# Kernel optimization log

Measured on AMD Instinct MI355X. Metric: run time of the kernel, lower is better.

## Reference

```python
import jax, jax.numpy as jnp
import numpy as np


def setup_inputs() -> dict:
    key = jax.random.key(0)
    k1, k2, k3, k4, k5 = jax.random.split(key, 5)
    B, D, H, W, C = 2, 16, 16, 16, 256
    x = jax.random.normal(k1, (B, D, H, W, C), dtype=jnp.float32)
    Wf = jax.random.normal(k2, (C, C // 4), dtype=jnp.float32) * (1.0 / np.sqrt(C))
    Wg = jax.random.normal(k3, (C, C // 4), dtype=jnp.float32) * (1.0 / np.sqrt(C))
    Wh = jax.random.normal(k4, (C, C), dtype=jnp.float32) * (1.0 / np.sqrt(C))
    gamma = jax.random.normal(k5, (1,), dtype=jnp.float32) * 0.1
    return {"x": x, "Wf": Wf, "Wg": Wg, "Wh": Wh, "gamma": gamma}


def reference(x, Wf, Wg, Wh, gamma):
    B, D, H, W, C = x.shape
    N = D * H * W
    xf = x.reshape(B, N, C)  # hw_flatten of input (1x1x1 conv == per-position matmul)
    f = jnp.einsum('bnc,cf->bnf', xf, Wf)   # [B, N, C//4]
    g = jnp.einsum('bnc,cf->bnf', xf, Wg)   # [B, N, C//4]
    h = jnp.einsum('bnc,cf->bnf', xf, Wh)   # [B, N, C]
    s = jnp.einsum('bnf,bmf->bnm', g, f)    # g @ f^T, [B, N, N]
    beta = jax.nn.softmax(s, axis=-1)
    o = jnp.einsum('bnm,bmc->bnc', beta, h)  # [B, N, C]
    out = gamma * o.reshape(B, D, H, W, C) + x
    beta_out = beta.reshape(-1, D, H, W, 1)  # [B*N, D, H, W, 1] as in original
    return (out, beta_out)
```

## Files before the change

### kernel.cpp

```cpp
#include <hip/hip_runtime.h>

#define NPOS 4096
#define CDIM 256
#define FDIM 64

typedef short short8 __attribute__((ext_vector_type(8)));
typedef float f32x4 __attribute__((ext_vector_type(4)));

__device__ __forceinline__ unsigned short f2bf(float v) {
  unsigned u = __float_as_uint(v);
  unsigned r = (u + 0x7fffu + ((u >> 16) & 1u)) >> 16;
  return (unsigned short)r;
}
__device__ __forceinline__ float bf2f(unsigned short u) {
  return __uint_as_float((unsigned)u << 16);
}
__device__ __forceinline__ short8 as_s8(uint4 u) {
  return *reinterpret_cast<short8*>(&u);
}
__device__ __forceinline__ void gload_lds16(const void* g, void* l) {
  __builtin_amdgcn_global_load_lds(
      (const __attribute__((address_space(1))) unsigned int*)g,
      (__attribute__((address_space(3))) unsigned int*)l, 16, 0, 0);
}

__global__ __launch_bounds__(256) void proj_kernel(
    const float* __restrict__ x, const float* __restrict__ Wf,
    const float* __restrict__ Wg, const float* __restrict__ Wh,
    unsigned short* __restrict__ f_hi, unsigned short* __restrict__ f_lo,
    unsigned short* __restrict__ g_hi, unsigned short* __restrict__ g_lo,
    unsigned short* __restrict__ h_t, float* __restrict__ out) {
  __shared__ float xs[16][CDIM];
  const int row0 = blockIdx.x * 16;
  const int t = threadIdx.x;
  {
    const float4* xv = reinterpret_cast<const float4*>(x + (size_t)row0 * CDIM);
    float4* sv = reinterpret_cast<float4*>(&xs[0][0]);
    float4* ov = reinterpret_cast<float4*>(out + (size_t)row0 * CDIM);
#pragma unroll
    for (int i = 0; i < 4; ++i) {
      const float4 v = xv[t + 256 * i];
      sv[t + 256 * i] = v;
      ov[t + 256 * i] = v;
    }
  }
  __syncthreads();
  {
    float acc[16];
#pragma unroll
    for (int r = 0; r < 16; ++r) acc[r] = 0.f;
    for (int k = 0; k < CDIM; k += 4) {
      const float w0 = Wh[(size_t)(k + 0) * CDIM + t];
      const float w1 = Wh[(size_t)(k + 1) * CDIM + t];
      const float w2 = Wh[(size_t)(k + 2) * CDIM + t];
      const float w3 = Wh[(size_t)(k + 3) * CDIM + t];
#pragma unroll
      for (int r = 0; r < 16; ++r) {
        const float4 xv = *reinterpret_cast<const float4*>(&xs[r][k]);
        float a = acc[r];
        a = fmaf(xv.x, w0, a);
        a = fmaf(xv.y, w1, a);
        a = fmaf(xv.z, w2, a);
        a = fmaf(xv.w, w3, a);
        acc[r] = a;
      }
    }
    const int b = row0 >> 12;
    const int lr = row0 & (NPOS - 1);
    unsigned wd[8];
#pragma unroll
    for (int i = 0; i < 8; ++i)
      wd[i] = (unsigned)f2bf(acc[2 * i]) | ((unsigned)f2bf(acc[2 * i + 1]) << 16);
    uint4* base = reinterpret_cast<uint4*>(h_t + ((size_t)(b * CDIM + t)) * NPOS);
    const int m = t & 7;
    const int c0 = lr >> 3;
    base[c0 ^ m] = make_uint4(wd[0], wd[1], wd[2], wd[3]);
    base[(c0 + 1) ^ m] = make_uint4(wd[4], wd[5], wd[6], wd[7]);
  }
  {
    const int col = t & 63;
    const int rb = (t >> 6) * 4;
    const int colq = col >> 3, cwi = col & 7;
    float af[4] = {0.f, 0.f, 0.f, 0.f};
    float ag[4] = {0.f, 0.f, 0.f, 0.f};
    for (int k = 0; k < CDIM; k += 4) {
      const float wf0 = Wf[(size_t)(k + 0) * FDIM + col];
      const float wf1 = Wf[(size_t)(k + 1) * FDIM + col];
      const float wf2 = Wf[(size_t)(k + 2) * FDIM + col];
      const float wf3 = Wf[(size_t)(k + 3) * FDIM + col];
      const float wg0 = Wg[(size_t)(k + 0) * FDIM + col];
      const float wg1 = Wg[(size_t)(k + 1) * FDIM + col];
      const float wg2 = Wg[(size_t)(k + 2) * FDIM + col];
      const float wg3 = Wg[(size_t)(k + 3) * FDIM + col];
#pragma unroll
      for (int r = 0; r < 4; ++r) {
        const float4 xv = *reinterpret_cast<const float4*>(&xs[rb + r][k]);
        float a = af[r], bb = ag[r];
        a = fmaf(xv.x, wf0, a); a = fmaf(xv.y, wf1, a);
        a = fmaf(xv.z, wf2, a); a = fmaf(xv.w, wf3, a);
        bb = fmaf(xv.x, wg0, bb); bb = fmaf(xv.y, wg1, bb);
        bb = fmaf(xv.z, wg2, bb); bb = fmaf(xv.w, wg3, bb);
        af[r] = a; ag[r] = bb;
      }
    }
#pragma unroll
    for (int r = 0; r < 4; ++r) {
      const int row = row0 + rb + r;
      const int ph = ((colq ^ (row & 7)) << 3) | cwi;
      const size_t of = (size_t)row * FDIM + ph;
      const size_t og = (size_t)row * FDIM + col;
      const unsigned short fh = f2bf(af[r]);
      const unsigned short gh = f2bf(ag[r]);
      f_hi[of] = fh;
      f_lo[of] = f2bf(af[r] - bf2f(fh));
      g_hi[og] = gh;
      g_lo[og] = f2bf(ag[r] - bf2f(gh));
    }
  }
}

__global__ __launch_bounds__(1024, 4) void qk_l_kernel(
    const unsigned short* __restrict__ f_hi, const unsigned short* __restrict__ f_lo,
    const unsigned short* __restrict__ g_hi, const unsigned short* __restrict__ g_lo,
    unsigned short* __restrict__ Pws, float* __restrict__ lrow) {
  __shared__ uint4 Fh[2][256][8];
  __shared__ uint4 Fl[2][256][8];
  __shared__ float partl[16][32];

  const int wg = blockIdx.x;
  const int wgid = (wg & 7) * 32 + (wg >> 3);
  const int b = wgid >> 7;
  const int row0 = (wgid & 127) * 32;
  const int t = threadIdx.x;
  const int w = t >> 6;
  const int l = t & 63;
  const int lr = l & 15;
  const int lk = l >> 4;

  short8 gh0[2], gl0[2], gh1[2], gl1[2];
  {
    const unsigned short* gH0 = g_hi + ((size_t)(b * NPOS + row0 + lr)) * FDIM + lk * 8;
    const unsigned short* gL0 = g_lo + ((size_t)(b * NPOS + row0 + lr)) * FDIM + lk * 8;
    const unsigned short* gH1 = gH0 + (size_t)16 * FDIM;
    const unsigned short* gL1 = gL0 + (size_t)16 * FDIM;
#pragma unroll
    for (int ks = 0; ks < 2; ++ks) {
      gh0[ks] = *reinterpret_cast<const short8*>(gH0 + ks * 32);
      gl0[ks] = *reinterpret_cast<const short8*>(gL0 + ks * 32);
      gh1[ks] = *reinterpret_cast<const short8*>(gH1 + ks * 32);
      gl1[ks] = *reinterpret_cast<const short8*>(gL1 + ks * 32);
    }
  }
  const unsigned short* fbh = f_hi + (size_t)b * NPOS * FDIM;
  const unsigned short* fbl = f_lo + (size_t)b * NPOS * FDIM;
  unsigned short* prow0 = Pws + (size_t)(b * NPOS + row0 + lr) * NPOS;
  unsigned short* prow1 = prow0 + (size_t)16 * NPOS;
  const int rsw = lr & 7;
  float lsum0 = 0.f, lsum1 = 0.f;

#define STAGEA(buf, tile)                                                      \
  do {                                                                         \
    _Pragma("unroll")                                                          \
    for (int j = 0; j < 2; ++j) {                                              \
      const int slot_ = j * 1024 + t;                                          \
      const int row_ = slot_ >> 3, ch_ = slot_ & 7;                            \
      gload_lds16(fbh + (size_t)((tile) * 256 + row_) * FDIM + ch_ * 8,        \
                  (char*)&Fh[buf][0][0] + (size_t)slot_ * 16);                 \
      gload_lds16(fbl + (size_t)((tile) * 256 + row_) * FDIM + ch_ * 8,        \
                  (char*)&Fl[buf][0][0] + (size_t)slot_ * 16);                 \
    }                                                                          \
  } while (0)

  STAGEA(0, 0);
  asm volatile("s_waitcnt vmcnt(0) lgkmcnt(0)\ns_barrier" ::: "memory");

  const int rrA = w * 16 + lr;
  const int fsw = rrA & 7;
  int buf = 0;
  for (int tile = 0; tile < 16; ++tile) {
    if (tile < 15) STAGEA(buf ^ 1, tile + 1);
    __builtin_amdgcn_sched_barrier(0);
    const uint4 h0 = Fh[buf][rrA][lk ^ fsw];
    const uint4 h1 = Fh[buf][rrA][(lk + 4) ^ fsw];
    const uint4 q0 = Fl[buf][rrA][lk ^ fsw];
    const uint4 q1 = Fl[buf][rrA][(lk + 4) ^ fsw];
    {
      f32x4 acca = {0.f, 0.f, 0.f, 0.f};
      f32x4 accb = {0.f, 0.f, 0.f, 0.f};
      acca = __builtin_amdgcn_mfma_f32_16x16x32_bf16(as_s8(h0), gh0[0], acca, 0, 0, 0);
      accb = __builtin_amdgcn_mfma_f32_16x16x32_bf16(as_s8(h0), gl0[0], accb, 0, 0, 0);
      acca = __builtin_amdgcn_mfma_f32_16x16x32_bf16(as_s8(q0), gh0[0], acca, 0, 0, 0);
      accb = __builtin_amdgcn_mfma_f32_16x16x32_bf16(as_s8(h1), gh0[1], accb, 0, 0, 0);
      acca = __builtin_amdgcn_mfma_f32_16x16x32_bf16(as_s8(q1), gh0[1], acca, 0, 0, 0);
      accb = __builtin_amdgcn_mfma_f32_16x16x32_bf16(as_s8(h1), gl0[1], accb, 0, 0, 0);
      const f32x4 acc = acca + accb;
      const int cq = tile * 256 + w * 16 + lk * 4;
      const float e0 = __expf(acc[0]);
      const float e1 = __expf(acc[1]);
      const float e2 = __expf(acc[2]);
      const float e3 = __expf(acc[3]);
      lsum0 += (e0 + e1) + (e2 + e3);
      uint2 pk;
      pk.x = (unsigned)f2bf(e0) | ((unsigned)f2bf(e1) << 16);
      pk.y = (unsigned)f2bf(e2) | ((unsigned)f2bf(e3) << 16);
      const int sidx = (((cq >> 3) ^ rsw) << 3) | (cq & 7);
      *reinterpret_cast<uint2*>(prow0 + sidx) = pk;
    }
    {
      f32x4 acca = {0.f, 0.f, 0.f, 0.f};
      f32x4 accb = {0.f, 0.f, 0.f, 0.f};
      acca = __builtin_amdgcn_mfma_f32_16x16x32_bf16(as_s8(h0), gh1[0], acca, 0, 0, 0);
      accb = __builtin_amdgcn_mfma_f32_16x16x32_bf16(as_s8(h0), gl1[0], accb, 0, 0, 0);
      acca = __builtin_amdgcn_mfma_f32_16x16x32_bf16(as_s8(q0), gh1[0], acca, 0, 0, 0);
      accb = __builtin_amdgcn_mfma_f32_16x16x32_bf16(as_s8(h1), gh1[1], accb, 0, 0, 0);
      acca = __builtin_amdgcn_mfma_f32_16x16x32_bf16(as_s8(q1), gh1[1], acca, 0, 0, 0);
      accb = __builtin_amdgcn_mfma_f32_16x16x32_bf16(as_s8(h1), gl1[1], accb, 0, 0, 0);
      const f32x4 acc = acca + accb;
      const int cq = tile * 256 + w * 16 + lk * 4;
      const float e0 = __expf(acc[0]);
      const float e1 = __expf(acc[1]);
      const float e2 = __expf(acc[2]);
      const float e3 = __expf(acc[3]);
      lsum1 += (e0 + e1) + (e2 + e3);
      uint2 pk;
      pk.x = (unsigned)f2bf(e0) | ((unsigned)f2bf(e1) << 16);
      pk.y = (unsigned)f2bf(e2) | ((unsigned)f2bf(e3) << 16);
      const int sidx = (((cq >> 3) ^ rsw) << 3) | (cq & 7);
      *reinterpret_cast<uint2*>(prow1 + sidx) = pk;
    }
    asm volatile("s_waitcnt vmcnt(2) lgkmcnt(0)\ns_barrier" ::: "memory");
    buf ^= 1;
  }
#undef STAGEA

  lsum0 += __shfl_xor(lsum0, 16);
  lsum0 += __shfl_xor(lsum0, 32);
  lsum1 += __shfl_xor(lsum1, 16);
  lsum1 += __shfl_xor(lsum1, 32);
  if (l < 16) {
    partl[w][l] = lsum0;
    partl[w][16 + l] = lsum1;
  }
  __syncthreads();
  if (t < 32) {
    float s = 0.f;
#pragma unroll
    for (int q = 0; q < 16; ++q) s += partl[q][t];
    lrow[(size_t)b * NPOS + row0 + t] = s;
  }
}

__global__ __launch_bounds__(1024, 4) void pv_split_kernel(
    const unsigned short* __restrict__ h_t, const unsigned short* __restrict__ Pws,
    const float* __restrict__ lrow, const float* __restrict__ gamma,
    float* __restrict__ beta, float* __restrict__ out, float* __restrict__ opart) {
  __shared__ uint4 Ab[2][64][8];
  __shared__ uint4 Bb[2][256][8];
  __shared__ float linvB[64];

  const int wg = blockIdx.x;
  const int wgid = (wg & 7) * 32 + (wg >> 3);
  const int b = wgid >> 7;
  const int khalf = (wgid >> 6) & 1;
  const int row0 = (wgid & 63) * 64;
  const int t = threadIdx.x;
  const int w = t >> 6;
  const int l = t & 63;
  const int lr = l & 15;
  const int lk = l >> 4;

  if (t < 64) linvB[t] = __frcp_rn(lrow[(size_t)b * NPOS + row0 + t]);

  const size_t hoff = (size_t)b * CDIM * NPOS;
  const unsigned short* Pb = Pws + (size_t)(b * NPOS + row0) * NPOS;
  const int kbase = khalf * 256;

#define STAGEB(bufi, kt)                                                        \
  do {                                                                          \
    _Pragma("unroll")                                                           \
    for (int j = 0; j < 2; ++j) {                                               \
      const int slot_ = j * 1024 + t;                                           \
      const int col_ = slot_ >> 3, ch_ = slot_ & 7;                             \
      const unsigned short* g_ = h_t + hoff + (size_t)col_ * NPOS +             \
                                 (size_t)(kbase + (kt) * 8 + ch_) * 8;          \
      gload_lds16(g_, (char*)&Bb[bufi][0][0] + (size_t)slot_ * 16);             \
    }                                                                           \
    if (t < 512) {                                                              \
      const int row_ = t >> 3, ch_ = t & 7;                                     \
      const unsigned short* g_ = Pb + (size_t)row_ * NPOS +                     \
                                 (size_t)(kbase + (kt) * 8 + ch_) * 8;          \
      gload_lds16(g_, (char*)&Ab[bufi][0][0] + (size_t)t * 16);                 \
    }                                                                           \
  } while (0)

  f32x4 acc0 = {0.f, 0.f, 0.f, 0.f}, acc1 = {0.f, 0.f, 0.f, 0.f};
  f32x4 acc2 = {0.f, 0.f, 0.f, 0.f}, acc3 = {0.f, 0.f, 0.f, 0.f};
  const int wrB = w & 3;
  const int wcB = w >> 2;
  const int arB = wrB * 16 + lr;
  const int c0 = wcB * 64 + lr;
  const int c1 = c0 + 16;
  const int c2 = c0 + 32;
  const int c3 = c0 + 48;
  const int brow = t >> 4;
  const int jj = t & 15;

  STAGEB(0, 0);
  asm volatile("s_waitcnt vmcnt(0) lgkmcnt(0)\ns_barrier" ::: "memory");
  const float il_brow = linvB[brow];

  int buf = 0;
  for (int kt = 0; kt < 32; ++kt) {
    if (kt < 31) STAGEB(buf ^ 1, kt + 1);
    __builtin_amdgcn_sched_barrier(0);
    {
      const uint4 a0 = Ab[buf][arB][lk ^ (arB & 7)];
      const uint4 a1 = Ab[buf][arB][(4 + lk) ^ (arB & 7)];
      const uint4 b00 = Bb[buf][c0][lk ^ (c0 & 7)];
      const uint4 b01 = Bb[buf][c1][lk ^ (c1 & 7)];
      const uint4 b02 = Bb[buf][c2][lk ^ (c2 & 7)];
      const uint4 b03 = Bb[buf][c3][lk ^ (c3 & 7)];
      acc0 = __builtin_amdgcn_mfma_f32_16x16x32_bf16(as_s8(a0), as_s8(b00), acc0, 0, 0, 0);
      acc1 = __builtin_amdgcn_mfma_f32_16x16x32_bf16(as_s8(a0), as_s8(b01), acc1, 0, 0, 0);
      acc2 = __builtin_amdgcn_mfma_f32_16x16x32_bf16(as_s8(a0), as_s8(b02), acc2, 0, 0, 0);
      acc3 = __builtin_amdgcn_mfma_f32_16x16x32_bf16(as_s8(a0), as_s8(b03), acc3, 0, 0, 0);
      const uint4 b10 = Bb[buf][c0][(4 + lk) ^ (c0 & 7)];
      const uint4 b11 = Bb[buf][c1][(4 + lk) ^ (c1 & 7)];
      const uint4 b12 = Bb[buf][c2][(4 + lk) ^ (c2 & 7)];
      const uint4 b13 = Bb[buf][c3][(4 + lk) ^ (c3 & 7)];
      acc0 = __builtin_amdgcn_mfma_f32_16x16x32_bf16(as_s8(a1), as_s8(b10), acc0, 0, 0, 0);
      acc1 = __builtin_amdgcn_mfma_f32_16x16x32_bf16(as_s8(a1), as_s8(b11), acc1, 0, 0, 0);
      acc2 = __builtin_amdgcn_mfma_f32_16x16x32_bf16(as_s8(a1), as_s8(b12), acc2, 0, 0, 0);
      acc3 = __builtin_amdgcn_mfma_f32_16x16x32_bf16(as_s8(a1), as_s8(b13), acc3, 0, 0, 0);
    }
    {
      const uint4 u4 = Ab[buf][brow][(jj >> 1) ^ (brow & 7)];
      const uint2 u = (jj & 1) ? make_uint2(u4.z, u4.w) : make_uint2(u4.x, u4.y);
      float4 v;
      v.x = bf2f((unsigned short)(u.x & 0xffffu)) * il_brow;
      v.y = bf2f((unsigned short)(u.x >> 16)) * il_brow;
      v.z = bf2f((unsigned short)(u.y & 0xffffu)) * il_brow;
      v.w = bf2f((unsigned short)(u.y >> 16)) * il_brow;
      *reinterpret_cast<float4*>(beta + (size_t)(b * NPOS + row0 + brow) * NPOS +
                                 khalf * 2048 + kt * 64 + jj * 4) = v;
    }
    asm volatile("s_waitcnt vmcnt(1) lgkmcnt(0)\ns_barrier" ::: "memory");
    buf ^= 1;
  }
#undef STAGEB

  const float gam = gamma[0];
  if (opart) {
    float* op = opart + (size_t)khalf * 2 * NPOS * CDIM;
#pragma unroll
    for (int r = 0; r < 4; ++r) {
      const int lrr = wrB * 16 + lk * 4 + r;
      const int orow = row0 + lrr;
      const float sc = gam * linvB[lrr];
      float* o = op + ((size_t)b * NPOS + orow) * CDIM + wcB * 64 + lr;
      o[0] = sc * acc0[r];
      o[16] = sc * acc1[r];
      o[32] = sc * acc2[r];
      o[48] = sc * acc3[r];
    }
  } else {
#pragma unroll
    for (int r = 0; r < 4; ++r) {
      const int lrr = wrB * 16 + lk * 4 + r;
      const int orow = row0 + lrr;
      const float sc = gam * linvB[lrr];
      float* o = out + ((size_t)b * NPOS + orow) * CDIM + wcB * 64 + lr;
      atomicAdd(o, sc * acc0[r]);
      atomicAdd(o + 16, sc * acc1[r]);
      atomicAdd(o + 32, sc * acc2[r]);
      atomicAdd(o + 48, sc * acc3[r]);
    }
  }
}

__global__ __launch_bounds__(256) void reduce_out_kernel(
    const float* __restrict__ x, const float* __restrict__ opart,
    float* __restrict__ out) {
  const size_t i = ((size_t)blockIdx.x * 256 + threadIdx.x) * 4;
  const float4 xv = *reinterpret_cast<const float4*>(x + i);
  const float4 a = *reinterpret_cast<const float4*>(opart + i);
  const float4 bq = *reinterpret_cast<const float4*>(opart + (size_t)2 * NPOS * CDIM + i);
  float4 r;
  r.x = xv.x + a.x + bq.x;
  r.y = xv.y + a.y + bq.y;
  r.z = xv.z + a.z + bq.z;
  r.w = xv.w + a.w + bq.w;
  *reinterpret_cast<float4*>(out + i) = r;
}

__global__ __launch_bounds__(1024, 4) void attn_fused_kernel(
    const unsigned short* __restrict__ f_hi, const unsigned short* __restrict__ f_lo,
    const unsigned short* __restrict__ g_hi, const unsigned short* __restrict__ g_lo,
    const unsigned short* __restrict__ h_t, const float* __restrict__ x,
    const float* __restrict__ gamma, float* __restrict__ beta,
    float* __restrict__ out) {
  __shared__ __align__(16) char shraw[110592];
  __shared__ float partl[16][16];
  __shared__ float linvs[32];
  uint4 (*Fh)[128][8] = reinterpret_cast<uint4(*)[128][8]>(shraw);
  uint4 (*Fl)[128][8] = reinterpret_cast<uint4(*)[128][8]>(shraw + 32768);
  uint4 (*Ab)[32][8] = reinterpret_cast<uint4(*)[32][8]>(shraw);
  uint4 (*Bb)[256][8] = reinterpret_cast<uint4(*)[256][8]>(shraw + 12288);

  const int wg = blockIdx.x;
  const int wgid = (wg & 7) * 32 + (wg >> 3);
  const int b = wgid >> 7;
  const int row0 = (wgid & 127) * 32;
  const int t = threadIdx.x;
  const int w = t >> 6;
  const int l = t & 63;
  const int lr = l & 15;
  const int lk = l >> 4;

  const int wr = w >> 3;
  const int wq = w & 7;
  const int arow = row0 + wr * 16 + lr;
  short8 gh[2], gl[2];
  {
    const unsigned short* gH = g_hi + ((size_t)(b * NPOS + arow)) * FDIM + lk * 8;
    const unsigned short* gL = g_lo + ((size_t)(b * NPOS + arow)) * FDIM + lk * 8;
#pragma unroll
    for (int ks = 0; ks < 2; ++ks) {
      gh[ks] = *reinterpret_cast<const short8*>(gH + ks * 32);
      gl[ks] = *reinterpret_cast<const short8*>(gL + ks * 32);
    }
  }
  const unsigned short* fbh = f_hi + (size_t)b * NPOS * FDIM;
  const unsigned short* fbl = f_lo + (size_t)b * NPOS * FDIM;
  unsigned short* Pb = (unsigned short*)(beta + (size_t)b * NPOS * NPOS);
  unsigned short* prow = Pb + (size_t)arow * (2 * NPOS) + NPOS;
  const int rsw = lr & 7;
  float lsum = 0.f;
  const int srow_ = t >> 3, sch_ = t & 7;

#define STAGEA(buf, tile)                                                      \
  do {                                                                         \
    const int tr_ = (tile) * 128 + srow_;                                      \
    gload_lds16(fbh + (size_t)tr_ * FDIM + sch_ * 8,                           \
                (char*)&Fh[buf][0][0] + (size_t)t * 16);                       \
    gload_lds16(fbl + (size_t)tr_ * FDIM + sch_ * 8,                           \
                (char*)&Fl[buf][0][0] + (size_t)t * 16);                       \
  } while (0)

  STAGEA(0, 0);
  asm volatile("s_waitcnt vmcnt(0) lgkmcnt(0)\ns_barrier" ::: "memory");

  const int rrA = wq * 16 + lr;
  const int fsw = rrA & 7;
  int buf = 0;
  for (int tile = 0; tile < 32; ++tile) {
    if (tile < 31) STAGEA(buf ^ 1, tile + 1);
    __builtin_amdgcn_sched_barrier(0);
    const uint4 h0 = Fh[buf][rrA][lk ^ fsw];
    const uint4 h1 = Fh[buf][rrA][(lk + 4) ^ fsw];
    const uint4 q0 = Fl[buf][rrA][lk ^ fsw];
    const uint4 q1 = Fl[buf][rrA][(lk + 4) ^ fsw];
    f32x4 acca = {0.f, 0.f, 0.f, 0.f};
    f32x4 accb = {0.f, 0.f, 0.f, 0.f};
    acca = __builtin_amdgcn_mfma_f32_16x16x32_bf16(as_s8(h0), gh[0], acca, 0, 0, 0);
    accb = __builtin_amdgcn_mfma_f32_16x16x32_bf16(as_s8(h0), gl[0], accb, 0, 0, 0);
    acca = __builtin_amdgcn_mfma_f32_16x16x32_bf16(as_s8(q0), gh[0], acca, 0, 0, 0);
    accb = __builtin_amdgcn_mfma_f32_16x16x32_bf16(as_s8(h1), gh[1], accb, 0, 0, 0);
    acca = __builtin_amdgcn_mfma_f32_16x16x32_bf16(as_s8(q1), gh[1], acca, 0, 0, 0);
    accb = __builtin_amdgcn_mfma_f32_16x16x32_bf16(as_s8(h1), gl[1], accb, 0, 0, 0);
    const f32x4 acc = acca + accb;
    const int cq = tile * 128 + wq * 16 + lk * 4;
    const float e0 = __expf(acc[0]);
    const float e1 = __expf(acc[1]);
    const float e2 = __expf(acc[2]);
    const float e3 = __expf(acc[3]);
    lsum += (e0 + e1) + (e2 + e3);
    uint2 pk;
    pk.x = (unsigned)f2bf(e0) | ((unsigned)f2bf(e1) << 16);
    pk.y = (unsigned)f2bf(e2) | ((unsigned)f2bf(e3) << 16);
    const int sidx = (((cq >> 3) ^ rsw) << 3) | (cq & 7);
    *reinterpret_cast<uint2*>(prow + sidx) = pk;
    asm volatile("s_waitcnt vmcnt(1) lgkmcnt(0)\ns_barrier" ::: "memory");
    buf ^= 1;
  }
#undef STAGEA

  lsum += __shfl_xor(lsum, 16);
  lsum += __shfl_xor(lsum, 32);
  if (l < 16) partl[w][l] = lsum;
  __syncthreads();
  if (t < 32) {
    const int half = t >> 4;
    float s = 0.f;
#pragma unroll
    for (int q = 0; q < 8; ++q) s += partl[half * 8 + q][t & 15];
    linvs[t] = __frcp_rn(s);
  }
  asm volatile("s_waitcnt vmcnt(0) lgkmcnt(0)\ns_barrier" ::: "memory");

  const size_t hoff = (size_t)b * CDIM * NPOS;
  const unsigned short* Pub = (const unsigned short*)(beta + (size_t)b * NPOS * NPOS);

#define STAGEB(bufi, kt)                                                        \
  do {                                                                          \
    {                                                                           \
      const int slot_ = w * 128 + l;                                            \
      const unsigned short* g_ = h_t + hoff + (size_t)(slot_ >> 3) * NPOS +     \
                                 (size_t)((kt) * 8 + (slot_ & 7)) * 8;          \
      gload_lds16(g_, (unsigned short*)&Bb[bufi][0][0] + (size_t)(w * 128) * 8);\
    }                                                                           \
    {                                                                           \
      const int slot_ = w * 128 + 64 + l;                                       \
      const unsigned short* g_ = h_t + hoff + (size_t)(slot_ >> 3) * NPOS +     \
                                 (size_t)((kt) * 8 + (slot_ & 7)) * 8;          \
      gload_lds16(g_, (unsigned short*)&Bb[bufi][0][0] +                        \
                          (size_t)(w * 128 + 64) * 8);                          \
    }                                                                           \
    if (t < 256) {                                                              \
      const unsigned short* g_ = Pub + (size_t)(row0 + (t >> 3)) * (2 * NPOS) + \
                                 NPOS + (size_t)((kt) * 8 + (t & 7)) * 8;       \
      gload_lds16(g_, (unsigned short*)&Ab[bufi][0][0] + (size_t)(w * 64) * 8); \
    }                                                                           \
  } while (0)

  f32x4 acc0 = {0.f, 0.f, 0.f, 0.f}, acc1 = {0.f, 0.f, 0.f, 0.f};
  const int wrB = w & 1;
  const int wcB = w >> 1;
  const int arB = wrB * 16 + lr;
  const int c0 = wcB * 32 + lr;
  const int c1 = c0 + 16;
  const int brow = t >> 5;
  const int jj = t & 31;
  const float il_brow = linvs[brow];

  STAGEB(0, 0);
  asm volatile("s_waitcnt vmcnt(0) lgkmcnt(0)\ns_barrier" ::: "memory");

  buf = 0;
  for (int kt = 0; kt < 64; ++kt) {
    if (kt < 63) STAGEB(buf ^ 1, kt + 1);
    __builtin_amdgcn_sched_barrier(0);
    {
      const uint4 a0 = Ab[buf][arB][lk ^ (arB & 7)];
      const uint4 a1 = Ab[buf][arB][(4 + lk) ^ (arB & 7)];
      const uint4 b00 = Bb[buf][c0][lk ^ (c0 & 7)];
      const uint4 b01 = Bb[buf][c1][lk ^ (c1 & 7)];
      const uint4 b10 = Bb[buf][c0][(4 + lk) ^ (c0 & 7)];
      const uint4 b11 = Bb[buf][c1][(4 + lk) ^ (c1 & 7)];
      acc0 = __builtin_amdgcn_mfma_f32_16x16x32_bf16(as_s8(a0), as_s8(b00), acc0, 0, 0, 0);
      acc1 = __builtin_amdgcn_mfma_f32_16x16x32_bf16(as_s8(a0), as_s8(b01), acc1, 0, 0, 0);
      acc0 = __builtin_amdgcn_mfma_f32_16x16x32_bf16(as_s8(a1), as_s8(b10), acc0, 0, 0, 0);
      acc1 = __builtin_amdgcn_mfma_f32_16x16x32_bf16(as_s8(a1), as_s8(b11), acc1, 0, 0, 0);
    }
    {
      const unsigned* arow_ = reinterpret_cast<const unsigned*>(&Ab[buf][brow][0]);
      const unsigned u = arow_[(((jj >> 2) ^ (brow & 7)) << 2) | (jj & 3)];
      float2 v;
      v.x = bf2f((unsigned short)(u & 0xffffu)) * il_brow;
      v.y = bf2f((unsigned short)(u >> 16)) * il_brow;
      *reinterpret_cast<float2*>(beta + (size_t)(b * NPOS + row0 + brow) * NPOS +
                                 (size_t)kt * 64 + jj * 2) = v;
    }
    asm volatile("s_waitcnt vmcnt(1) lgkmcnt(0)\ns_barrier" ::: "memory");
    buf ^= 1;
  }
#undef STAGEB

  const float gam = gamma[0];
#pragma unroll
  for (int r = 0; r < 4; ++r) {
    const int lrr = wrB * 16 + lk * 4 + r;
    const int orow = row0 + lrr;
    const float sc = gam * linvs[lrr];
    const size_t i0 = ((size_t)b * NPOS + orow) * CDIM + wcB * 32 + lr;
    out[i0] = fmaf(sc, acc0[r], x[i0]);
    out[i0 + 16] = fmaf(sc, acc1[r], x[i0 + 16]);
  }
}

extern "C" void kernel_launch(void* const* d_in, const int* in_sizes, int n_in,
                              void* d_out, int out_size, void* d_ws, size_t ws_size,
                              hipStream_t stream) {
  (void)in_sizes; (void)n_in; (void)out_size;
  const float* x = (const float*)d_in[0];
  const float* Wf = (const float*)d_in[1];
  const float* Wg = (const float*)d_in[2];
  const float* Wh = (const float*)d_in[3];
  const float* gamma = (const float*)d_in[4];

  float* out = (float*)d_out;
  float* beta = out + (size_t)2 * NPOS * CDIM;

  unsigned short* h_t = (unsigned short*)d_ws;
  unsigned short* f_hi = h_t + (size_t)2 * CDIM * NPOS;
  unsigned short* f_lo = f_hi + (size_t)2 * NPOS * FDIM;
  unsigned short* g_hi = f_lo + (size_t)2 * NPOS * FDIM;
  unsigned short* g_lo = g_hi + (size_t)2 * NPOS * FDIM;
  float* lrow = (float*)(g_lo + (size_t)2 * NPOS * FDIM);
  unsigned short* Pws = (unsigned short*)(lrow + 2 * NPOS);
  float* opart = (float*)(Pws + (size_t)2 * NPOS * NPOS);

  const size_t need = ((char*)opart) - (char*)d_ws;
  const size_t need2 = ((char*)(opart + (size_t)4 * NPOS * CDIM)) - (char*)d_ws;

  hipLaunchKernelGGL(proj_kernel, dim3(2 * NPOS / 16), dim3(256), 0, stream,
                     x, Wf, Wg, Wh, f_hi, f_lo, g_hi, g_lo, h_t, out);
  if (ws_size >= need2) {
    hipLaunchKernelGGL(qk_l_kernel, dim3(256), dim3(1024), 0, stream,
                       f_hi, f_lo, g_hi, g_lo, Pws, lrow);
    hipLaunchKernelGGL(pv_split_kernel, dim3(256), dim3(1024), 0, stream,
                       h_t, Pws, lrow, gamma, beta, out, opart);
    hipLaunchKernelGGL(reduce_out_kernel, dim3(2 * NPOS * CDIM / 1024), dim3(256),
                       0, stream, x, opart, out);
  } else if (ws_size >= need) {
    hipLaunchKernelGGL(qk_l_kernel, dim3(256), dim3(1024), 0, stream,
                       f_hi, f_lo, g_hi, g_lo, Pws, lrow);
    hipLaunchKernelGGL(pv_split_kernel, dim3(256), dim3(1024), 0, stream,
                       h_t, Pws, lrow, gamma, beta, out, nullptr);
  } else {
    hipLaunchKernelGGL(attn_fused_kernel, dim3(256), dim3(1024), 0, stream,
                       f_hi, f_lo, g_hi, g_lo, h_t, x, gamma, beta, out);
  }
}
```

Measured before the change: 121.9 us.

## Replace scalar projection with split-bf16 MFMA projection kernel and pre-split weights

Adds a small kernel that transposes Wf/Wg/Wh and splits them into bf16 hi/lo parts, then a new projection kernel that converts x tiles to hi/lo bf16 in LDS and computes f, g and h with three-term MFMA products. The scalar FP32 projection kernel is dropped from the main path. The aim is to move the projection GEMM onto matrix cores while keeping near-FP32 accuracy. The trade-off is one extra launch and about three times the MFMA work of plain bf16. The mid-size-workspace path is removed, and the fallback path now uses the old projection.

```diff
diff --git a/kernel.cpp b/kernel.cpp
--- a/kernel.cpp
+++ b/kernel.cpp
@@ -22,6 +22,140 @@
   __builtin_amdgcn_global_load_lds(
       (const __attribute__((address_space(1))) unsigned int*)g,
       (__attribute__((address_space(3))) unsigned int*)l, 16, 0, 0);
+}
+
+__global__ __launch_bounds__(256) void wsplit_kernel(
+    const float* __restrict__ Wf, const float* __restrict__ Wg,
+    const float* __restrict__ Wh, unsigned short* __restrict__ WThi,
+    unsigned short* __restrict__ WTlo) {
+  const int cw = blockIdx.x;
+  const int k = threadIdx.x;
+  float v;
+  if (cw < 64) v = Wf[(size_t)k * 64 + cw];
+  else if (cw < 128) v = Wg[(size_t)k * 64 + (cw - 64)];
+  else v = Wh[(size_t)k * 256 + (cw - 128)];
+  const unsigned short hi = f2bf(v);
+  WThi[(size_t)cw * 256 + k] = hi;
+  WTlo[(size_t)cw * 256 + k] = f2bf(v - bf2f(hi));
+}
+
+__global__ __launch_bounds__(1024, 4) void proj_mfma_kernel(
+    const float* __restrict__ x, const unsigned short* __restrict__ WThi,
+    const unsigned short* __restrict__ WTlo,
+    unsigned short* __restrict__ f_hi, unsigned short* __restrict__ f_lo,
+    unsigned short* __restrict__ g_hi, unsigned short* __restrict__ g_lo,
+    unsigned short* __restrict__ h_t) {
+  __shared__ uint4 Xh[32][32];
+  __shared__ uint4 Xl[32][32];
+  const int grow0 = blockIdx.x * 32;
+  const int bidx = grow0 >> 12;
+  const int t = threadIdx.x;
+  const int w = t >> 6;
+  const int l = t & 63;
+  const int lr = l & 15;
+  const int lk = l >> 4;
+
+  {
+    const int srow = t >> 5;
+    const int k0 = (t & 31) * 8;
+    const float* xp = x + (size_t)(grow0 + srow) * CDIM + k0;
+    const float4 v0 = *reinterpret_cast<const float4*>(xp);
+    const float4 v1 = *reinterpret_cast<const float4*>(xp + 4);
+    const unsigned short h0 = f2bf(v0.x), h1 = f2bf(v0.y), h2 = f2bf(v0.z),
+                         h3 = f2bf(v0.w), h4 = f2bf(v1.x), h5 = f2bf(v1.y),
+                         h6 = f2bf(v1.z), h7 = f2bf(v1.w);
+    uint4 ph, pl;
+    ph.x = (unsigned)h0 | ((unsigned)h1 << 16);
+    ph.y = (unsigned)h2 | ((unsigned)h3 << 16);
+    ph.z = (unsigned)h4 | ((unsigned)h5 << 16);
+    ph.w = (unsigned)h6 | ((unsigned)h7 << 16);
+    pl.x = (unsigned)f2bf(v0.x - bf2f(h0)) | ((unsigned)f2bf(v0.y - bf2f(h1)) << 16);
+    pl.y = (unsigned)f2bf(v0.z - bf2f(h2)) | ((unsigned)f2bf(v0.w - bf2f(h3)) << 16);
+    pl.z = (unsigned)f2bf(v1.x - bf2f(h4)) | ((unsigned)f2bf(v1.y - bf2f(h5)) << 16);
+    pl.w = (unsigned)f2bf(v1.z - bf2f(h6)) | ((unsigned)f2bf(v1.w - bf2f(h7)) << 16);
+    const int ch = (t & 31) ^ (srow & 7);
+    Xh[srow][ch] = ph;
+    Xl[srow][ch] = pl;
+  }
+  __syncthreads();
+
+#pragma unroll
+  for (int i = 0; i < 3; ++i) {
+    const int tau = w * 3 + i;
+    if (tau < 32) {
+      const int mt = tau >> 4;
+      const int nt = tau & 15;
+      const int arow = mt * 16 + lr;
+      const int asw = arow & 7;
+      const int cw = 128 + nt * 16 + lr;
+      const unsigned short* bh = WThi + (size_t)cw * 256 + lk * 8;
+      const unsigned short* bl = WTlo + (size_t)cw * 256 + lk * 8;
+      f32x4 acc = {0.f, 0.f, 0.f, 0.f};
+#pragma unroll
+      for (int ks = 0; ks < 8; ++ks) {
+        const int o = (ks * 4 + lk) ^ asw;
+        const uint4 ah = Xh[arow][o];
+        const uint4 al = Xl[arow][o];
+        const uint4 bhv = *reinterpret_cast<const uint4*>(bh + ks * 32);
+        const uint4 blv = *reinterpret_cast<const uint4*>(bl + ks * 32);
+        acc = __builtin_amdgcn_mfma_f32_16x16x32_bf16(as_s8(ah), as_s8(bhv), acc, 0, 0, 0);
+        acc = __builtin_amdgcn_mfma_f32_16x16x32_bf16(as_s8(al), as_s8(bhv), acc, 0, 0, 0);
+        acc = __builtin_amdgcn_mfma_f32_16x16x32_bf16(as_s8(ah), as_s8(blv), acc, 0, 0, 0);
+      }
+      const int col = nt * 16 + lr;
+      const int k0 = (grow0 & 4095) + mt * 16 + lk * 4;
+      const int phys = (((k0 >> 3) ^ (col & 7)) << 3) | (k0 & 7);
+      uint2 pk;
+      pk.x = (unsigned)f2bf(acc[0]) | ((unsigned)f2bf(acc[1]) << 16);
+      pk.y = (unsigned)f2bf(acc[2]) | ((unsigned)f2bf(acc[3]) << 16);
+      *reinterpret_cast<uint2*>(h_t + ((size_t)(bidx * CDIM + col)) * NPOS + phys) = pk;
+    } else {
+      const int tp = tau - 32;
+      const int mt = tp >> 1;
+      const int nt = tp & 1;
+      const int cw = mt * 16 + lr;
+      const unsigned short* ahp = WThi + (size_t)cw * 256 + lk * 8;
+      const unsigned short* alp = WTlo + (size_t)cw * 256 + lk * 8;
+      const int xrow = nt * 16 + lr;
+      const int xsw = xrow & 7;
+      f32x4 acc = {0.f, 0.f, 0.f, 0.f};
+#pragma unroll
+      for (int ks = 0; ks < 8; ++ks) {
+        const int o = (ks * 4 + lk) ^ xsw;
+        const uint4 ah = *reinterpret_cast<const uint4*>(ahp + ks * 32);
+        const uint4 al = *reinterpret_cast<const uint4*>(alp + ks * 32);
+        const uint4 bh = Xh[xrow][o];
+        const uint4 bl = Xl[xrow][o];
+        acc = __builtin_amdgcn_mfma_f32_16x16x32_bf16(as_s8(ah), as_s8(bh), acc, 0, 0, 0);
+        acc = __builtin_amdgcn_mfma_f32_16x16x32_bf16(as_s8(al), as_s8(bh), acc, 0, 0, 0);
+        acc = __builtin_amdgcn_mfma_f32_16x16x32_bf16(as_s8(ah), as_s8(bl), acc, 0, 0, 0);
+      }
+      const int xn = nt * 16 + lr;
+      const int grow = grow0 + xn;
+      const int wc0 = mt * 16 + lk * 4;
+      const unsigned short e0 = f2bf(acc[0]);
+      const unsigned short e1 = f2bf(acc[1]);
+      const unsigned short e2 = f2bf(acc[2]);
+      const unsigned short e3 = f2bf(acc[3]);
+      uint2 pkh, pkl;
+      pkh.x = (unsigned)e0 | ((unsigned)e1 << 16);
+      pkh.y = (unsigned)e2 | ((unsigned)e3 << 16);
+      pkl.x = (unsigned)f2bf(acc[0] - bf2f(e0)) |
+              ((unsigned)f2bf(acc[1] - bf2f(e1)) << 16);
+      pkl.y = (unsigned)f2bf(acc[2] - bf2f(e2)) |
+              ((unsigned)f2bf(acc[3] - bf2f(e3)) << 16);
+      if (wc0 < 64) {
+        const int cc = wc0;
+        const int phys = (((cc >> 3) ^ (grow & 7)) << 3) | (cc & 7);
+        *reinterpret_cast<uint2*>(f_hi + (size_t)grow * FDIM + phys) = pkh;
+        *reinterpret_cast<uint2*>(f_lo + (size_t)grow * FDIM + phys) = pkl;
+      } else {
+        const int cc = wc0 - 64;
+        *reinterpret_cast<uint2*>(g_hi + (size_t)grow * FDIM + cc) = pkh;
+        *reinterpret_cast<uint2*>(g_lo + (size_t)grow * FDIM + cc) = pkl;
+      }
+    }
+  }
 }
 
 __global__ __launch_bounds__(256) void proj_kernel(
@@ -597,27 +731,28 @@
   unsigned short* g_hi = f_lo + (size_t)2 * NPOS * FDIM;
   unsigned short* g_lo = g_hi + (size_t)2 * NPOS * FDIM;
   float* lrow = (float*)(g_lo + (size_t)2 * NPOS * FDIM);
-  unsigned short* Pws = (unsigned short*)(lrow + 2 * NPOS);
+  unsigned short* WThi = (unsigned short*)(lrow + 2 * NPOS);
+  unsigned short* WTlo = WThi + (size_t)384 * 256;
+  unsigned short* Pws = WTlo + (size_t)384 * 256;
   float* opart = (float*)(Pws + (size_t)2 * NPOS * NPOS);
 
-  const size_t need = ((char*)opart) - (char*)d_ws;
-  const size_t need2 = ((char*)(opart + (size_t)4 * NPOS * CDIM)) - (char*)d_ws;
-
-  hipLaunchKernelGGL(proj_kernel, dim3(2 * NPOS / 16), dim3(256), 0, stream,
-                     x, Wf, Wg, Wh, f_hi, f_lo, g_hi, g_lo, h_t, out);
-  if (ws_size >= need2) {
+  const size_t need_full =
+      ((char*)(opart + (size_t)4 * NPOS * CDIM)) - (char*)d_ws;
+
+  if (ws_size >= need_full) {
+    hipLaunchKernelGGL(wsplit_kernel, dim3(384), dim3(256), 0, stream,
+                       Wf, Wg, Wh, WThi, WTlo);
+    hipLaunchKernelGGL(proj_mfma_kernel, dim3(256), dim3(1024), 0, stream,
+                       x, WThi, WTlo, f_hi, f_lo, g_hi, g_lo, h_t);
     hipLaunchKernelGGL(qk_l_kernel, dim3(256), dim3(1024), 0, stream,
                        f_hi, f_lo, g_hi, g_lo, Pws, lrow);
     hipLaunchKernelGGL(pv_split_kernel, dim3(256), dim3(1024), 0, stream,
                        h_t, Pws, lrow, gamma, beta, out, opart);
     hipLaunchKernelGGL(reduce_out_kernel, dim3(2 * NPOS * CDIM / 1024), dim3(256),
                        0, stream, x, opart, out);
-  } else if (ws_size >= need) {
-    hipLaunchKernelGGL(qk_l_kernel, dim3(256), dim3(1024), 0, stream,
-                       f_hi, f_lo, g_hi, g_lo, Pws, lrow);
-    hipLaunchKernelGGL(pv_split_kernel, dim3(256), dim3(1024), 0, stream,
-                       h_t, Pws, lrow, gamma, beta, out, nullptr);
   } else {
+    hipLaunchKernelGGL(proj_kernel, dim3(2 * NPOS / 16), dim3(256), 0, stream,
+                       x, Wf, Wg, Wh, f_hi, f_lo, g_hi, g_lo, h_t, out);
     hipLaunchKernelGGL(attn_fused_kernel, dim3(256), dim3(1024), 0, stream,
                        f_hi, f_lo, g_hi, g_lo, h_t, x, gamma, beta, out);
   }
```

Measured after the change: 112.4 us. -7.8%, faster.
